# Performance work log

Hardware: AMD Instinct MI355X
Metric: run time of the kernel (lower is better)

## Reference

```python
import jax, jax.numpy as jnp
import numpy as np

H = 16
D_MODEL = 1024
D_HID = 50  # hidden width of the 1->50->1 mask MLP


def setup_inputs() -> dict:
    key = jax.random.key(0)
    ks = jax.random.split(key, 16)
    B, S, D = 16, 768, D_MODEL
    n, nk = 512, 256  # code length n, redundancy n-k; S = n + nk
    inp = {
        "query": jax.random.normal(ks[0], (B, S, D), jnp.float32),
        "key": jax.random.normal(ks[1], (B, S, D), jnp.float32),
        "value": jax.random.normal(ks[2], (B, S, D), jnp.float32),
        "pc_matrix": jax.random.uniform(ks[3], (nk, n), jnp.float32),
        # four Linear(d_model, d_model) layers: q, k, v, out. Stored so that y = x @ W + b.
        "Wq": jax.random.normal(ks[4], (D, D), jnp.float32) * 0.02,
        "bq": jnp.zeros((D,), jnp.float32),
        "Wk": jax.random.normal(ks[5], (D, D), jnp.float32) * 0.02,
        "bk": jnp.zeros((D,), jnp.float32),
        "Wv": jax.random.normal(ks[6], (D, D), jnp.float32) * 0.02,
        "bv": jnp.zeros((D,), jnp.float32),
        "Wo": jax.random.normal(ks[7], (D, D), jnp.float32) * 0.02,
        "bo": jnp.zeros((D,), jnp.float32),
        # one_d_mapping: Linear(1,50) -> ReLU -> Linear(50,1)
        "mw1": jax.random.normal(ks[8], (1, D_HID), jnp.float32) * 0.5,
        "mb1": jax.random.normal(ks[9], (D_HID,), jnp.float32) * 0.1,
        "mw2": jax.random.normal(ks[10], (D_HID, 1), jnp.float32) * 0.5,
        "mb2": jnp.zeros((1,), jnp.float32),
    }
    return inp


def _mask_from_pc(pc, mw1, mb1, mw2, mb2):
    # pc: (nk, n). Build (S, S) block matrix, S = n + nk.
    nknk = pc @ pc.T            # (nk, nk)
    nn = pc.T @ pc              # (n, n)
    top = jnp.concatenate([nn, pc.T], axis=1)     # (n, S)
    bot = jnp.concatenate([pc, nknk], axis=1)     # (nk, S)
    M = jnp.concatenate([top, bot], axis=0)       # (S, S)
    # elementwise 1->50->1 MLP
    h = jax.nn.relu(M[..., None] * mw1[0] + mb1)  # (S, S, 50)
    out = h @ mw2 + mb2                           # (S, S, 1)
    return out[..., 0]                            # (S, S)


def reference(query, key, value, pc_matrix, Wq, bq, Wk, bk, Wv, bv, Wo, bo,
              mw1, mb1, mw2, mb2):
    B, S, D = query.shape
    dk = D // H
    q = (query @ Wq + bq).reshape(B, S, H, dk).transpose(0, 2, 1, 3)
    k = (key @ Wk + bk).reshape(B, S, H, dk).transpose(0, 2, 1, 3)
    v = (value @ Wv + bv).reshape(B, S, H, dk).transpose(0, 2, 1, 3)
    scores = jnp.einsum("bhqd,bhkd->bhqk", q, k) / jnp.sqrt(jnp.float32(dk))
    mask = _mask_from_pc(pc_matrix, mw1, mb1, mw2, mb2)  # (S, S)
    scores = scores * mask[None, None]  # multiplicative float mask
    p = jax.nn.softmax(scores, axis=-1)  # dropout is identity in eval mode
    x = jnp.einsum("bhqk,bhkd->bhqd", p, v)
    x = x.transpose(0, 2, 1, 3).reshape(B, S, D)
    return x @ Wo + bo
```

## Files before the change

### kernel.cpp

```cpp
#include <hip/hip_runtime.h>
#include <stdint.h>

typedef _Float16 f16;
typedef _Float16 f16x8 __attribute__((ext_vector_type(8)));
typedef float f32x4 __attribute__((ext_vector_type(4)));

union U4 { uint4 u; f16 h[8]; };

#define GLOAD16(g, l)                                                         \
  __builtin_amdgcn_global_load_lds(                                           \
      (const __attribute__((address_space(1))) void*)(g),                     \
      (__attribute__((address_space(3))) void*)(l), 16, 0, 0)

__global__ __launch_bounds__(256) void k_wt(const float* __restrict__ W0,
                                            const float* __restrict__ W1,
                                            const float* __restrict__ W2,
                                            const float* __restrict__ W3,
                                            f16* __restrict__ T0, f16* __restrict__ T1,
                                            f16* __restrict__ T2, f16* __restrict__ T3) {
    __shared__ f16 tile[64 * 65];
    int z = blockIdx.z;
    const float* W = z == 0 ? W0 : z == 1 ? W1 : z == 2 ? W2 : W3;
    f16* Wt = z == 0 ? T0 : z == 1 ? T1 : z == 2 ? T2 : T3;
    int t = threadIdx.x;
    int k0 = blockIdx.x * 64, n0 = blockIdx.y * 64;
    #pragma unroll
    for (int i = 0; i < 4; i++) {
        int cid = t + i * 256;
        int row = cid >> 4, c4 = cid & 15;
        float4 v = *(const float4*)(W + (size_t)(k0 + row) * 1024 + n0 + c4 * 4);
        tile[(c4 * 4 + 0) * 65 + row] = (f16)v.x;
        tile[(c4 * 4 + 1) * 65 + row] = (f16)v.y;
        tile[(c4 * 4 + 2) * 65 + row] = (f16)v.z;
        tile[(c4 * 4 + 3) * 65 + row] = (f16)v.w;
    }
    __syncthreads();
    #pragma unroll
    for (int i = 0; i < 2; i++) {
        int cid = t + i * 256;
        int nr = cid >> 3, kc = cid & 7;
        U4 u;
        #pragma unroll
        for (int j = 0; j < 8; j++) u.h[j] = tile[nr * 65 + kc * 8 + j];
        *(uint4*)(Wt + (size_t)(n0 + nr) * 1024 + k0 + kc * 8) = u.u;
    }
}

__global__ __launch_bounds__(256) void k_cvt(const float* __restrict__ in,
                                             f16* __restrict__ out) {
    size_t id = (size_t)blockIdx.x * 256 + threadIdx.x;
    float4 a = *(const float4*)(in + id * 8);
    float4 b = *(const float4*)(in + id * 8 + 4);
    U4 u;
    u.h[0] = (f16)a.x; u.h[1] = (f16)a.y; u.h[2] = (f16)a.z; u.h[3] = (f16)a.w;
    u.h[4] = (f16)b.x; u.h[5] = (f16)b.y; u.h[6] = (f16)b.z; u.h[7] = (f16)b.w;
    *(uint4*)(out + id * 8) = u.u;
}

template <int TRANS>
__global__ __launch_bounds__(256) void k_gram(const float* __restrict__ pc,
                                              float* __restrict__ out) {
    constexpr int N = TRANS ? 256 : 512;
    constexpr int K = TRANS ? 512 : 256;
    __shared__ float As[16][68];
    __shared__ float Bs[16][68];
    int t = threadIdx.x;
    int i0 = blockIdx.x * 64, j0 = blockIdx.y * 64;
    int ty = t >> 4, tx = t & 15;
    float acc[4][4];
    #pragma unroll
    for (int r = 0; r < 4; r++)
        #pragma unroll
        for (int c = 0; c < 4; c++) acc[r][c] = 0.f;

    for (int kt = 0; kt < K; kt += 16) {
        if (TRANS == 0) {
            int k = t >> 4, c4 = t & 15;
            float4 va = *(const float4*)(pc + (size_t)(kt + k) * 512 + i0 + c4 * 4);
            float4 vb = *(const float4*)(pc + (size_t)(kt + k) * 512 + j0 + c4 * 4);
            *(float4*)&As[k][c4 * 4] = va;
            *(float4*)&Bs[k][c4 * 4] = vb;
        } else {
            int r = t >> 2, kc = t & 3;
            float4 va = *(const float4*)(pc + (size_t)(i0 + r) * 512 + kt + kc * 4);
            As[kc * 4 + 0][r] = va.x; As[kc * 4 + 1][r] = va.y;
            As[kc * 4 + 2][r] = va.z; As[kc * 4 + 3][r] = va.w;
            float4 vb = *(const float4*)(pc + (size_t)(j0 + r) * 512 + kt + kc * 4);
            Bs[kc * 4 + 0][r] = vb.x; Bs[kc * 4 + 1][r] = vb.y;
            Bs[kc * 4 + 2][r] = vb.z; Bs[kc * 4 + 3][r] = vb.w;
        }
        __syncthreads();
        #pragma unroll
        for (int u = 0; u < 16; u++) {
            float4 av = *(const float4*)&As[u][ty * 4];
            float4 bv = *(const float4*)&Bs[u][tx * 4];
            float aa[4] = {av.x, av.y, av.z, av.w};
            float bb[4] = {bv.x, bv.y, bv.z, bv.w};
            #pragma unroll
            for (int r = 0; r < 4; r++)
                #pragma unroll
                for (int c = 0; c < 4; c++) acc[r][c] += aa[r] * bb[c];
        }
        __syncthreads();
    }
    #pragma unroll
    for (int r = 0; r < 4; r++)
        #pragma unroll
        for (int c = 0; c < 4; c++)
            out[(size_t)(i0 + ty * 4 + r) * N + j0 + tx * 4 + c] = acc[r][c];
}

__global__ __launch_bounds__(256) void k_mask(const float* __restrict__ pc,
                                              const float* __restrict__ nn,
                                              const float* __restrict__ nknk,
                                              const float* __restrict__ mw1,
                                              const float* __restrict__ mb1,
                                              const float* __restrict__ mw2,
                                              const float* __restrict__ mb2,
                                              float* __restrict__ maskp) {
    __shared__ float w1[50], b1[50], w2[50];
    int t = threadIdx.x;
    if (t < 50) { w1[t] = mw1[t]; b1[t] = mb1[t]; w2[t] = mw2[t]; }
    __syncthreads();
    int id = blockIdx.x * 256 + t;
    int i = id / 768, j = id - i * 768;
    float M;
    if (i < 512) M = (j < 512) ? nn[(size_t)i * 512 + j] : pc[(size_t)(j - 512) * 512 + i];
    else         M = (j < 512) ? pc[(size_t)(i - 512) * 512 + j]
                               : nknk[(size_t)(i - 512) * 256 + (j - 512)];
    float acc = mb2[0];
    #pragma unroll 10
    for (int u = 0; u < 50; u++) acc += fmaxf(M * w1[u] + b1[u], 0.f) * w2[u];
    maskp[id] = acc;
}

__global__ __launch_bounds__(256) void k_vt(const f16* __restrict__ Vh,
                                            f16* __restrict__ VT) {
    __shared__ f16 tile[64][72];
    int t = threadIdx.x;
    int s0 = blockIdx.x * 64;
    int bh = blockIdx.y, b = bh >> 4, h = bh & 15;
    #pragma unroll
    for (int p = 0; p < 2; p++) {
        int cid = t + p * 256;
        int s = cid >> 3, dc = cid & 7;
        *(uint4*)&tile[s][dc * 8] =
            *(const uint4*)(Vh + ((size_t)b * 768 + s0 + s) * 1024 + h * 64 + dc * 8);
    }
    __syncthreads();
    #pragma unroll
    for (int p = 0; p < 2; p++) {
        int cid = t + p * 256;
        int d = cid >> 3, sc = cid & 7;
        U4 u;
        #pragma unroll
        for (int j = 0; j < 8; j++) u.h[j] = tile[sc * 8 + j][d];
        *(uint4*)(VT + ((size_t)bh * 64 + d) * 768 + s0 + sc * 8) = u.u;
    }
}

template <int MODE>
__global__ __launch_bounds__(256) void k_gemm(const f16* __restrict__ A,
                                              const f16* __restrict__ Bt,
                                              const float* __restrict__ bias,
                                              void* out0v, void* out1v) {
    __shared__ f16 As[128 * 32];
    __shared__ f16 Bs[128 * 32];
    int t = threadIdx.x;
    int w = t >> 6, lane = t & 63, l15 = lane & 15, quad = lane >> 4;
    int wm = w >> 1, wn = w & 1;
    int id = blockIdx.x;
    int rest = id >> 3;
    int row0 = ((id & 7) * 12 + rest % 12) * 128;
    int n0 = (rest / 12) * 128;

    int m0 = w * 16 + (lane >> 2);
    int m1 = m0 + 64;
    int ks0 = (lane & 3) ^ ((m0 >> 1) & 3);
    int ks1 = (lane & 3) ^ ((m1 >> 1) & 3);
    const f16* gA0 = A + (size_t)(row0 + m0) * 1024 + ks0 * 8;
    const f16* gA1 = A + (size_t)(row0 + m1) * 1024 + ks1 * 8;
    const f16* gB0 = Bt + (size_t)(n0 + m0) * 1024 + ks0 * 8;
    const f16* gB1 = Bt + (size_t)(n0 + m1) * 1024 + ks1 * 8;
    f16* lA = As + w * 512;
    f16* lB = Bs + w * 512;
    int sw = (l15 >> 1) & 3;

    f32x4 acc[4][4];
    #pragma unroll
    for (int mi = 0; mi < 4; mi++)
        #pragma unroll
        for (int ni = 0; ni < 4; ni++) acc[mi][ni] = (f32x4){0.f, 0.f, 0.f, 0.f};

    for (int kt = 0; kt < 32; kt++) {
        int k0 = kt * 32;
        GLOAD16(gA0 + k0, lA);
        GLOAD16(gA1 + k0, lA + 2048);
        GLOAD16(gB0 + k0, lB);
        GLOAD16(gB1 + k0, lB + 2048);
        __syncthreads();
        f16x8 af[4], bf_[4];
        #pragma unroll
        for (int mi = 0; mi < 4; mi++)
            af[mi] = *(const f16x8*)((const char*)As +
                     (size_t)(wm * 64 + mi * 16 + l15) * 64 + ((quad ^ sw) << 4));
        #pragma unroll
        for (int ni = 0; ni < 4; ni++)
            bf_[ni] = *(const f16x8*)((const char*)Bs +
                      (size_t)(wn * 64 + ni * 16 + l15) * 64 + ((quad ^ sw) << 4));
        #pragma unroll
        for (int mi = 0; mi < 4; mi++)
            #pragma unroll
            for (int ni = 0; ni < 4; ni++)
                acc[mi][ni] = __builtin_amdgcn_mfma_f32_16x16x32_f16(af[mi], bf_[ni],
                                                                     acc[mi][ni], 0, 0, 0);
        __syncthreads();
    }
    #pragma unroll
    for (int mi = 0; mi < 4; mi++) {
        #pragma unroll
        for (int ni = 0; ni < 4; ni++) {
            int col = n0 + wn * 64 + ni * 16 + l15;
            float bv = bias[col];
            #pragma unroll
            for (int r = 0; r < 4; r++) {
                int row = row0 + wm * 64 + mi * 16 + quad * 4 + r;
                float v = acc[mi][ni][r] + bv;
                size_t idx = (size_t)row * 1024 + col;
                if (MODE == 0) {
                    ((f16*)out0v)[idx] = (f16)v;
                } else if (MODE == 1) {
                    f16 hi = (f16)v;
                    ((f16*)out0v)[idx] = hi;
                    ((f16*)out1v)[idx] = (f16)(v - (float)hi);
                } else {
                    ((float*)out0v)[idx] = v;
                }
            }
        }
    }
}

__global__ __launch_bounds__(256) void k_attn(const f16* __restrict__ Qhi,
                                              const f16* __restrict__ Qlo,
                                              const f16* __restrict__ Khi,
                                              const f16* __restrict__ Klo,
                                              const f16* __restrict__ VT,
                                              const float* __restrict__ maskp,
                                              f16* __restrict__ Xout) {
    __shared__ f16 Ksh[2][64 * 64];
    __shared__ f16 Ksl[2][64 * 64];
    __shared__ f16 Vs[2][64 * 64];
    __shared__ f16 Ps[4][16 * 64];
    int t = threadIdx.x;
    int w = t >> 6, lane = t & 63, l15 = lane & 15, quad = lane >> 4;
    int id = blockIdx.x;
    int bh = (id & 7) + ((id >> 3) / 12) * 8;
    int q0 = ((id >> 3) % 12) * 64;
    int b = bh >> 4, h = bh & 15;
    const size_t base = ((size_t)b * 768) * 1024 + h * 64;

    int srow = lane >> 3;
    int sslot = lane & 7;

    f16x8 qh[2], ql[2];
    int qrow = q0 + w * 16 + l15;
    #pragma unroll
    for (int c = 0; c < 2; c++) {
        qh[c] = *(const f16x8*)(Qhi + base + (size_t)qrow * 1024 + c * 32 + quad * 8);
        ql[c] = *(const f16x8*)(Qlo + base + (size_t)qrow * 1024 + c * 32 + quad * 8);
    }
    float mst[4], lst[4];
    f32x4 o[4];
    #pragma unroll
    for (int r = 0; r < 4; r++) { mst[r] = -1e30f; lst[r] = 0.f; }
    #pragma unroll
    for (int ni = 0; ni < 4; ni++) o[ni] = (f32x4){0.f, 0.f, 0.f, 0.f};

    auto STAGE = [&](int bsel, int k0) {
        #pragma unroll
        for (int p = 0; p < 2; p++) {
            int row = w * 16 + p * 8 + srow;
            int ss = sslot ^ (row & 7);
            GLOAD16(Khi + base + (size_t)(k0 + row) * 1024 + ss * 8,
                    &Ksh[bsel][w * 1024 + p * 512]);
            GLOAD16(Klo + base + (size_t)(k0 + row) * 1024 + ss * 8,
                    &Ksl[bsel][w * 1024 + p * 512]);
            GLOAD16(VT + ((size_t)bh * 64 + row) * 768 + k0 + ss * 8,
                    &Vs[bsel][w * 1024 + p * 512]);
        }
    };

    STAGE(0, 0);
    __syncthreads();
    int buf = 0;
    int kx = l15 & 7;

    for (int kt = 0; kt < 12; kt++) {
        int k0 = kt * 64;
        float mv[4][4];
        #pragma unroll
        for (int kn = 0; kn < 4; kn++)
            #pragma unroll
            for (int r = 0; r < 4; r++)
                mv[kn][r] = maskp[(q0 + w * 16 + quad * 4 + r) * 768 + k0 + kn * 16 + l15];
        if (kt < 11) STAGE(buf ^ 1, k0 + 64);

        float sv[4][4];
        #pragma unroll
        for (int kn = 0; kn < 4; kn++) {
            f32x4 s = (f32x4){0.f, 0.f, 0.f, 0.f};
            int key = kn * 16 + l15;
            #pragma unroll
            for (int c = 0; c < 2; c++) {
                int slot = ((c << 2) + quad) ^ kx;
                f16x8 kh = *(const f16x8*)((const char*)&Ksh[buf][0] +
                                           (size_t)key * 128 + (slot << 4));
                f16x8 kl = *(const f16x8*)((const char*)&Ksl[buf][0] +
                                           (size_t)key * 128 + (slot << 4));
                s = __builtin_amdgcn_mfma_f32_16x16x32_f16(qh[c], kh, s, 0, 0, 0);
                s = __builtin_amdgcn_mfma_f32_16x16x32_f16(ql[c], kh, s, 0, 0, 0);
                s = __builtin_amdgcn_mfma_f32_16x16x32_f16(qh[c], kl, s, 0, 0, 0);
            }
            #pragma unroll
            for (int r = 0; r < 4; r++) sv[kn][r] = s[r] * 0.125f * mv[kn][r];
        }

        float tmr[4];
        bool need = false;
        #pragma unroll
        for (int r = 0; r < 4; r++) {
            float tm = fmaxf(fmaxf(sv[0][r], sv[1][r]), fmaxf(sv[2][r], sv[3][r]));
            tm = fmaxf(tm, __shfl_xor(tm, 1));
            tm = fmaxf(tm, __shfl_xor(tm, 2));
            tm = fmaxf(tm, __shfl_xor(tm, 4));
            tm = fmaxf(tm, __shfl_xor(tm, 8));
            tmr[r] = tm;
            need = need || (tm > mst[r] + 8.f);
        }
        if (__any(need)) {
            #pragma unroll
            for (int r = 0; r < 4; r++) {
                float mn = fmaxf(mst[r], tmr[r]);
                float alpha = __expf(mst[r] - mn);
                mst[r] = mn;
                lst[r] *= alpha;
                #pragma unroll
                for (int ni = 0; ni < 4; ni++) o[ni][r] *= alpha;
            }
        }
        #pragma unroll
        for (int r = 0; r < 4; r++) {
            int row = quad * 4 + r;
            float p0 = __expf(sv[0][r] - mst[r]);
            float p1 = __expf(sv[1][r] - mst[r]);
            float p2 = __expf(sv[2][r] - mst[r]);
            float p3 = __expf(sv[3][r] - mst[r]);
            float rs = (p0 + p1) + (p2 + p3);
            rs += __shfl_xor(rs, 1);
            rs += __shfl_xor(rs, 2);
            rs += __shfl_xor(rs, 4);
            rs += __shfl_xor(rs, 8);
            lst[r] += rs;
            int rl = l15 >> 3, re = l15 & 7, rx = row & 7;
            Ps[w][row * 64 + ((0 + rl) ^ rx) * 8 + re] = (f16)p0;
            Ps[w][row * 64 + ((2 + rl) ^ rx) * 8 + re] = (f16)p1;
            Ps[w][row * 64 + ((4 + rl) ^ rx) * 8 + re] = (f16)p2;
            Ps[w][row * 64 + ((6 + rl) ^ rx) * 8 + re] = (f16)p3;
        }
        asm volatile("s_waitcnt lgkmcnt(0)" ::: "memory");
        #pragma unroll
        for (int c = 0; c < 2; c++) {
            int pslot = ((c << 2) + quad) ^ kx;
            f16x8 pa = *(const f16x8*)((const char*)&Ps[w][0] +
                                       (size_t)l15 * 128 + (pslot << 4));
            #pragma unroll
            for (int ni = 0; ni < 4; ni++) {
                int d = ni * 16 + l15;
                f16x8 vb = *(const f16x8*)((const char*)&Vs[buf][0] +
                                           (size_t)d * 128 + (pslot << 4));
                o[ni] = __builtin_amdgcn_mfma_f32_16x16x32_f16(pa, vb, o[ni], 0, 0, 0);
            }
        }
        __syncthreads();
        buf ^= 1;
    }
    #pragma unroll
    for (int ni = 0; ni < 4; ni++)
        #pragma unroll
        for (int r = 0; r < 4; r++) {
            int row = q0 + w * 16 + quad * 4 + r;
            int col = ni * 16 + l15;
            Xout[((size_t)b * 768 + row) * 1024 + h * 64 + col] = (f16)(o[ni][r] / lst[r]);
        }
}

extern "C" void kernel_launch(void* const* d_in, const int* in_sizes, int n_in,
                              void* d_out, int out_size, void* d_ws, size_t ws_size,
                              hipStream_t stream) {
    (void)in_sizes; (void)n_in; (void)out_size; (void)ws_size;
    const float* query = (const float*)d_in[0];
    const float* key   = (const float*)d_in[1];
    const float* value = (const float*)d_in[2];
    const float* pc    = (const float*)d_in[3];
    const float* Wq    = (const float*)d_in[4];
    const float* bq    = (const float*)d_in[5];
    const float* Wk    = (const float*)d_in[6];
    const float* bk    = (const float*)d_in[7];
    const float* Wv    = (const float*)d_in[8];
    const float* bv    = (const float*)d_in[9];
    const float* Wo    = (const float*)d_in[10];
    const float* bo    = (const float*)d_in[11];
    const float* mw1   = (const float*)d_in[12];
    const float* mb1   = (const float*)d_in[13];
    const float* mw2   = (const float*)d_in[14];
    const float* mb2   = (const float*)d_in[15];

    char* p = (char*)d_ws;
    auto take = [&](size_t bytes) -> char* {
        char* r = p; p += (bytes + 255) & ~(size_t)255; return r;
    };
    const size_t NTOK = 12288, DM = 1024;
    float* maskb = (float*)take(768 * 768 * 4);
    float* nnb   = (float*)take(512 * 512 * 4);
    float* nknkb = (float*)take(256 * 256 * 4);
    f16* Wqt = (f16*)take(DM * DM * 2);
    f16* Wkt = (f16*)take(DM * DM * 2);
    f16* Wvt = (f16*)take(DM * DM * 2);
    f16* Wot = (f16*)take(DM * DM * 2);
    f16* buf1 = (f16*)take(NTOK * DM * 2);
    f16* Qhi = (f16*)take(NTOK * DM * 2);
    f16* Qlo = (f16*)take(NTOK * DM * 2);
    f16* Khi = (f16*)take(NTOK * DM * 2);
    f16* Klo = (f16*)take(NTOK * DM * 2);
    f16* Vhb = (f16*)take(NTOK * DM * 2);
    f16* VTb = (f16*)take(NTOK * DM * 2);

    k_wt<<<dim3(16, 16, 4), 256, 0, stream>>>(Wq, Wk, Wv, Wo, Wqt, Wkt, Wvt, Wot);
    k_gram<0><<<dim3(8, 8), 256, 0, stream>>>(pc, nnb);
    k_gram<1><<<dim3(4, 4), 256, 0, stream>>>(pc, nknkb);
    k_mask<<<2304, 256, 0, stream>>>(pc, nnb, nknkb, mw1, mb1, mw2, mb2, maskb);

    k_cvt<<<6144, 256, 0, stream>>>(query, buf1);
    k_gemm<1><<<768, 256, 0, stream>>>(buf1, Wqt, bq, Qhi, Qlo);
    k_cvt<<<6144, 256, 0, stream>>>(key, buf1);
    k_gemm<1><<<768, 256, 0, stream>>>(buf1, Wkt, bk, Khi, Klo);
    k_cvt<<<6144, 256, 0, stream>>>(value, buf1);
    k_gemm<0><<<768, 256, 0, stream>>>(buf1, Wvt, bv, Vhb, nullptr);

    k_vt<<<dim3(12, 256), 256, 0, stream>>>(Vhb, VTb);

    k_attn<<<3072, 256, 0, stream>>>(Qhi, Qlo, Khi, Klo, VTb, maskb, buf1);

    k_gemm<2><<<768, 256, 0, stream>>>(buf1, Wot, bo, d_out, nullptr);
}
```

Measured before the change: 631.0 us.

## Transpose attention MFMA layout so each lane owns one query row

```diff
diff --git a/kernel.cpp b/kernel.cpp
--- a/kernel.cpp
+++ b/kernel.cpp
@@ -6,6 +6,7 @@
 typedef float f32x4 __attribute__((ext_vector_type(4)));
 
 union U4 { uint4 u; f16 h[8]; };
+union U2 { uint2 u; f16 h[4]; };
 
 #define GLOAD16(g, l)                                                         \
   __builtin_amdgcn_global_load_lds(                                           \
@@ -131,7 +132,7 @@
     float acc = mb2[0];
     #pragma unroll 10
     for (int u = 0; u < 50; u++) acc += fmaxf(M * w1[u] + b1[u], 0.f) * w2[u];
-    maskp[id] = acc;
+    maskp[id] = acc * 0.18033688011112042f;
 }
 
 __global__ __launch_bounds__(256) void k_vt(const f16* __restrict__ Vh,
@@ -270,10 +271,8 @@
         qh[c] = *(const f16x8*)(Qhi + base + (size_t)qrow * 1024 + c * 32 + quad * 8);
         ql[c] = *(const f16x8*)(Qlo + base + (size_t)qrow * 1024 + c * 32 + quad * 8);
     }
-    float mst[4], lst[4];
+    float mrow = -1e30f, lrow = 0.f;
     f32x4 o[4];
-    #pragma unroll
-    for (int r = 0; r < 4; r++) { mst[r] = -1e30f; lst[r] = 0.f; }
     #pragma unroll
     for (int ni = 0; ni < 4; ni++) o[ni] = (f32x4){0.f, 0.f, 0.f, 0.f};
 
@@ -295,15 +294,16 @@
     __syncthreads();
     int buf = 0;
     int kx = l15 & 7;
+    const float* mbase = maskp + (size_t)quad * 4 * 768 + q0 + w * 16 + l15;
 
     for (int kt = 0; kt < 12; kt++) {
         int k0 = kt * 64;
-        float mv[4][4];
+        float mvs[4][4];
         #pragma unroll
         for (int kn = 0; kn < 4; kn++)
             #pragma unroll
             for (int r = 0; r < 4; r++)
-                mv[kn][r] = maskp[(q0 + w * 16 + quad * 4 + r) * 768 + k0 + kn * 16 + l15];
+                mvs[kn][r] = mbase[(size_t)(k0 + kn * 16 + r) * 768];
         if (kt < 11) STAGE(buf ^ 1, k0 + 64);
 
         float sv[4][4];
@@ -318,57 +318,50 @@
                                            (size_t)key * 128 + (slot << 4));
                 f16x8 kl = *(const f16x8*)((const char*)&Ksl[buf][0] +
                                            (size_t)key * 128 + (slot << 4));
-                s = __builtin_amdgcn_mfma_f32_16x16x32_f16(qh[c], kh, s, 0, 0, 0);
-                s = __builtin_amdgcn_mfma_f32_16x16x32_f16(ql[c], kh, s, 0, 0, 0);
-                s = __builtin_amdgcn_mfma_f32_16x16x32_f16(qh[c], kl, s, 0, 0, 0);
+                s = __builtin_amdgcn_mfma_f32_16x16x32_f16(kh, qh[c], s, 0, 0, 0);
+                s = __builtin_amdgcn_mfma_f32_16x16x32_f16(kh, ql[c], s, 0, 0, 0);
+                s = __builtin_amdgcn_mfma_f32_16x16x32_f16(kl, qh[c], s, 0, 0, 0);
             }
             #pragma unroll
-            for (int r = 0; r < 4; r++) sv[kn][r] = s[r] * 0.125f * mv[kn][r];
-        }
-
-        float tmr[4];
-        bool need = false;
-        #pragma unroll
-        for (int r = 0; r < 4; r++) {
-            float tm = fmaxf(fmaxf(sv[0][r], sv[1][r]), fmaxf(sv[2][r], sv[3][r]));
-            tm = fmaxf(tm, __shfl_xor(tm, 1));
-            tm = fmaxf(tm, __shfl_xor(tm, 2));
-            tm = fmaxf(tm, __shfl_xor(tm, 4));
-            tm = fmaxf(tm, __shfl_xor(tm, 8));
-            tmr[r] = tm;
-            need = need || (tm > mst[r] + 8.f);
-        }
-        if (__any(need)) {
+            for (int r = 0; r < 4; r++) sv[kn][r] = s[r] * mvs[kn][r];
+        }
+
+        float tk0 = fmaxf(fmaxf(sv[0][0], sv[0][1]), fmaxf(sv[0][2], sv[0][3]));
+        float tk1 = fmaxf(fmaxf(sv[1][0], sv[1][1]), fmaxf(sv[1][2], sv[1][3]));
+        float tk2 = fmaxf(fmaxf(sv[2][0], sv[2][1]), fmaxf(sv[2][2], sv[2][3]));
+        float tk3 = fmaxf(fmaxf(sv[3][0], sv[3][1]), fmaxf(sv[3][2], sv[3][3]));
+        float tm = fmaxf(fmaxf(tk0, tk1), fmaxf(tk2, tk3));
+        tm = fmaxf(tm, __shfl_xor(tm, 16));
+        tm = fmaxf(tm, __shfl_xor(tm, 32));
+        if (__any(tm > mrow + 11.0f)) {
+            float mn = fmaxf(mrow, tm);
+            float alpha = exp2f(mrow - mn);
+            mrow = mn;
+            lrow *= alpha;
+            #pragma unroll
+            for (int ni = 0; ni < 4; ni++)
+                #pragma unroll
+                for (int r = 0; r < 4; r++) o[ni][r] *= alpha;
+        }
+        float rs = 0.f;
+        #pragma unroll
+        for (int kn = 0; kn < 4; kn++) {
+            U2 pk;
             #pragma unroll
             for (int r = 0; r < 4; r++) {
-                float mn = fmaxf(mst[r], tmr[r]);
-                float alpha = __expf(mst[r] - mn);
-                mst[r] = mn;
-                lst[r] *= alpha;
-                #pragma unroll
-                for (int ni = 0; ni < 4; ni++) o[ni][r] *= alpha;
+                float pv = exp2f(sv[kn][r] - mrow);
+                rs += pv;
+                pk.h[r] = (f16)pv;
             }
-        }
-        #pragma unroll
-        for (int r = 0; r < 4; r++) {
-            int row = quad * 4 + r;
-            float p0 = __expf(sv[0][r] - mst[r]);
-            float p1 = __expf(sv[1][r] - mst[r]);
-            float p2 = __expf(sv[2][r] - mst[r]);
-            float p3 = __expf(sv[3][r] - mst[r]);
-            float rs = (p0 + p1) + (p2 + p3);
-            rs += __shfl_xor(rs, 1);
-            rs += __shfl_xor(rs, 2);
-            rs += __shfl_xor(rs, 4);
-            rs += __shfl_xor(rs, 8);
-            lst[r] += rs;
-            int rl = l15 >> 3, re = l15 & 7, rx = row & 7;
-            Ps[w][row * 64 + ((0 + rl) ^ rx) * 8 + re] = (f16)p0;
-            Ps[w][row * 64 + ((2 + rl) ^ rx) * 8 + re] = (f16)p1;
-            Ps[w][row * 64 + ((4 + rl) ^ rx) * 8 + re] = (f16)p2;
-            Ps[w][row * 64 + ((6 + rl) ^ rx) * 8 + re] = (f16)p3;
-        }
+            int slot = (kn * 2 + (quad >> 1)) ^ kx;
+            *(uint2*)((char*)&Ps[w][0] + l15 * 128 + (slot << 4) + ((quad & 1) << 3)) = pk.u;
+        }
+        rs += __shfl_xor(rs, 16);
+        rs += __shfl_xor(rs, 32);
+        lrow += rs;
+
         asm volatile("s_waitcnt lgkmcnt(0)" ::: "memory");
+        __builtin_amdgcn_sched_barrier(0);
         #pragma unroll
         for (int c = 0; c < 2; c++) {
             int pslot = ((c << 2) + quad) ^ kx;
@@ -379,20 +372,21 @@
                 int d = ni * 16 + l15;
                 f16x8 vb = *(const f16x8*)((const char*)&Vs[buf][0] +
                                            (size_t)d * 128 + (pslot << 4));
-                o[ni] = __builtin_amdgcn_mfma_f32_16x16x32_f16(pa, vb, o[ni], 0, 0, 0);
+                o[ni] = __builtin_amdgcn_mfma_f32_16x16x32_f16(vb, pa, o[ni], 0, 0, 0);
             }
         }
         __syncthreads();
         buf ^= 1;
     }
-    #pragma unroll
-    for (int ni = 0; ni < 4; ni++)
-        #pragma unroll
-        for (int r = 0; r < 4; r++) {
-            int row = q0 + w * 16 + quad * 4 + r;
-            int col = ni * 16 + l15;
-            Xout[((size_t)b * 768 + row) * 1024 + h * 64 + col] = (f16)(o[ni][r] / lst[r]);
-        }
+    float rl = 1.0f / lrow;
+    int qg = q0 + w * 16 + l15;
+    #pragma unroll
+    for (int ni = 0; ni < 4; ni++) {
+        U2 ok;
+        #pragma unroll
+        for (int r = 0; r < 4; r++) ok.h[r] = (f16)(o[ni][r] * rl);
+        *(uint2*)(Xout + ((size_t)b * 768 + qg) * 1024 + h * 64 + ni * 16 + quad * 4) = ok.u;
+    }
 }
 
 extern "C" void kernel_launch(void* const* d_in, const int* in_sizes, int n_in,
```

Measured after the change: 606.6 us. 1.04x faster.
